# Kernel tuning notes

Hardware: AMD Instinct MI355X
Metric: run time of the kernel (lower is better)

The kernel has to match this reference:

```python
import jax, jax.numpy as jnp
import numpy as np

H = 1024      # hidden_size
NH = 16       # n_heads
DK = 64       # d_kv


def setup_inputs() -> dict:
    key = jax.random.key(0)
    k1, k2, k3, k4, k5 = jax.random.split(key, 5)
    x = jax.random.normal(k1, (4, 2048, H), dtype=jnp.float32)
    # dense1: hidden -> 3*n_heads*d_kv
    W1 = jax.random.normal(k2, (H, 3 * NH * DK), dtype=jnp.float32) / np.sqrt(H)
    b1 = jax.random.normal(k3, (3 * NH * DK,), dtype=jnp.float32) * 0.02
    # dense2: n_heads*d_kv -> hidden
    W2 = jax.random.normal(k4, (NH * DK, H), dtype=jnp.float32) / np.sqrt(NH * DK)
    b2 = jax.random.normal(k5, (H,), dtype=jnp.float32) * 0.02
    return {"x": x, "W1": W1, "b1": b1, "W2": W2, "b2": b2}


def reference(x, W1, b1, W2, b2):
    B, S, _ = x.shape
    scale = 1.0 / np.sqrt(DK)
    qkv = x @ W1 + b1                                   # [B,S,3*NH*DK]
    qkv = qkv.reshape(B, S, 3, NH, DK)
    q, k, v = jnp.moveaxis(qkv, 2, 0)                   # each [B,S,NH,DK]
    q = q.transpose(0, 2, 1, 3)                         # [B,NH,S,DK]
    k = k.transpose(0, 2, 1, 3)
    v = v.transpose(0, 2, 1, 3)
    scores = jnp.einsum('bhqd,bhkd->bhqk', q, k) * scale  # [B,NH,S,S]
    attn = jax.nn.softmax(scores, axis=-1)
    ctx = jnp.einsum('bhqk,bhkd->bhqd', attn, v)        # [B,NH,S,DK]
    ctx = ctx.transpose(0, 2, 1, 3).reshape(B, S, NH * DK)
    return ctx @ W2 + b2
```

## Files before the change

### kernel.cpp

```cpp
#include <hip/hip_runtime.h>
#include <hip/hip_bf16.h>


typedef __hip_bfloat16 bf16;
typedef __attribute__((ext_vector_type(8))) short bf16x8;
typedef __attribute__((ext_vector_type(4))) float f32x4;

#define B_   4
#define S_   2048
#define H_   1024
#define NH_  16
#define DK_  64
#define M_   8192
#define N1_  3072
#define K_   1024

#define SCALE_Q 0.18033688f

typedef const __attribute__((address_space(1))) void* gas_t;
typedef __attribute__((address_space(3))) void* las_t;
#define G2L16(g, l) __builtin_amdgcn_global_load_lds((gas_t)(g), (las_t)(l), 16, 0, 0)

__device__ __forceinline__ float b2f(bf16 v) { return __bfloat162float(v); }

__device__ __forceinline__ unsigned pk2(float a, float b) {
    unsigned ua = __float_as_uint(a);
    unsigned ub = __float_as_uint(b);
    ua += 0x7FFFu + ((ua >> 16) & 1u);
    ub += 0x7FFFu + ((ub >> 16) & 1u);
    return (ua >> 16) | (ub & 0xFFFF0000u);
}

__global__ __launch_bounds__(256) void conv_x(const float* __restrict__ X,
                                              bf16* __restrict__ Xb)
{
    size_t i = ((size_t)blockIdx.x * 256 + threadIdx.x) * 8;
    float4 lo = *(const float4*)&X[i];
    float4 hi = *(const float4*)&X[i + 4];
    uint4 u;
    u.x = pk2(lo.x, lo.y); u.y = pk2(lo.z, lo.w);
    u.z = pk2(hi.x, hi.y); u.w = pk2(hi.z, hi.w);
    *(uint4*)&Xb[i] = u;
}

__global__ __launch_bounds__(256) void conv_wT(const float* __restrict__ W,
                                               bf16* __restrict__ WT,
                                               int Kdim, int Ndim)
{
    __shared__ bf16 T[64][72];
    const int tid = threadIdx.x;
    const int n0 = blockIdx.x * 64, k0 = blockIdx.y * 64;
    const int kr = tid >> 4, nc = (tid & 15) * 4;
    #pragma unroll
    for (int p = 0; p < 4; ++p) {
        float4 v = *(const float4*)&W[(size_t)(k0 + kr + p * 16) * Ndim + n0 + nc];
        T[nc + 0][kr + p * 16] = __float2bfloat16(v.x);
        T[nc + 1][kr + p * 16] = __float2bfloat16(v.y);
        T[nc + 2][kr + p * 16] = __float2bfloat16(v.z);
        T[nc + 3][kr + p * 16] = __float2bfloat16(v.w);
    }
    __syncthreads();
    const int nr = tid >> 2, kc = (tid & 3) * 16;
    *(bf16x8*)&WT[(size_t)(n0 + nr) * Kdim + k0 + kc]     = *(const bf16x8*)&T[nr][kc];
    *(bf16x8*)&WT[(size_t)(n0 + nr) * Kdim + k0 + kc + 8] = *(const bf16x8*)&T[nr][kc + 8];
}

__device__ __forceinline__ void qkv_epilogue(
    const f32x4 acc[4][4], const float* __restrict__ B1,
    bf16* __restrict__ Qp, bf16* __restrict__ Kp, bf16* __restrict__ Vt,
    int n0, int m0, int wm, int wn, int quad, int col)
{
    const int which = n0 >> 10;
    const int bb = m0 >> 11;
    if (which == 2) {
        #pragma unroll
        for (int i = 0; i < 4; ++i) {
            int s = (m0 & (S_ - 1)) + wm * 64 + i * 16 + quad * 4;
            #pragma unroll
            for (int j = 0; j < 4; ++j) {
                int n = n0 + wn * 64 + j * 16 + col;
                int h = (n >> 6) & 15, d = n & 63;
                float bv = B1[n];
                uint2 t;
                t.x = pk2(acc[i][j][0] + bv, acc[i][j][1] + bv);
                t.y = pk2(acc[i][j][2] + bv, acc[i][j][3] + bv);
                *(uint2*)&Vt[(((size_t)(bb * NH_ + h)) * DK_ + d) * S_ + s] = t;
            }
        }
    } else {
        bf16* dst = which ? Kp : Qp;
        const float sc = which ? 1.0f : SCALE_Q;
        #pragma unroll
        for (int i = 0; i < 4; ++i) {
            #pragma unroll
            for (int r = 0; r < 4; ++r) {
                int s = (m0 & (S_ - 1)) + wm * 64 + i * 16 + quad * 4 + r;
                #pragma unroll
                for (int j = 0; j < 4; ++j) {
                    int n = n0 + wn * 64 + j * 16 + col;
                    int h = (n >> 6) & 15, d = n & 63;
                    dst[(((size_t)(bb * NH_ + h)) * S_ + s) * DK_ + d] =
                        __float2bfloat16((acc[i][j][r] + B1[n]) * sc);
                }
            }
        }
    }
}

__global__ __launch_bounds__(256) void gemm_qkv_mfma2(
    const bf16* __restrict__ Xb, const bf16* __restrict__ W1T,
    const float* __restrict__ B1,
    bf16* __restrict__ Qp, bf16* __restrict__ Kp, bf16* __restrict__ Vt)
{
    __shared__ bf16 As[128 * 32];
    __shared__ bf16 Bs[128 * 32];

    const int tid = threadIdx.x;
    const int lane = tid & 63, wv = tid >> 6;
    const int col = lane & 15, quad = lane >> 4;
    const int wm = wv >> 1, wn = wv & 1;
    const int n0 = blockIdx.x * 128, m0 = blockIdx.y * 128;

    f32x4 acc[4][4] = {};

    const bf16* Ag = Xb  + (size_t)m0 * K_;
    const bf16* Bg = W1T + (size_t)n0 * K_;

    for (int k0 = 0; k0 < K_; k0 += 32) {
        #pragma unroll
        for (int h = 0; h < 2; ++h) {
            int idx = tid + h * 256;
            int row = idx >> 2, c = (idx & 3) * 8;
            G2L16(Ag + (size_t)row * K_ + k0 + c, As + (size_t)idx * 8);
            G2L16(Bg + (size_t)row * K_ + k0 + c, Bs + (size_t)idx * 8);
        }
        __syncthreads();

        bf16x8 af[4], bfr[4];
        #pragma unroll
        for (int i = 0; i < 4; ++i)
            af[i] = *(const bf16x8*)&As[(wm * 64 + i * 16 + col) * 32 + quad * 8];
        #pragma unroll
        for (int j = 0; j < 4; ++j)
            bfr[j] = *(const bf16x8*)&Bs[(wn * 64 + j * 16 + col) * 32 + quad * 8];

        #pragma unroll
        for (int i = 0; i < 4; ++i)
            #pragma unroll
            for (int j = 0; j < 4; ++j)
                acc[i][j] = __builtin_amdgcn_mfma_f32_16x16x32_bf16(af[i], bfr[j], acc[i][j], 0, 0, 0);
        __syncthreads();
    }
    qkv_epilogue(acc, B1, Qp, Kp, Vt, n0, m0, wm, wn, quad, col);
}

__global__ __launch_bounds__(256) void gemm_qkv_mfma(
    const float* __restrict__ X, const bf16* __restrict__ W1T,
    const float* __restrict__ B1,
    bf16* __restrict__ Qp, bf16* __restrict__ Kp, bf16* __restrict__ Vt)
{
    __shared__ bf16 As[128 * 32];
    __shared__ bf16 Bs[128 * 32];

    const int tid = threadIdx.x;
    const int lane = tid & 63, wv = tid >> 6;
    const int col = lane & 15, quad = lane >> 4;
    const int wm = wv >> 1, wn = wv & 1;
    const int n0 = blockIdx.x * 128, m0 = blockIdx.y * 128;

    f32x4 acc[4][4] = {};

    const float* Ag = X   + (size_t)m0 * K_;
    const bf16*  Bg = W1T + (size_t)n0 * K_;

    for (int k0 = 0; k0 < K_; k0 += 32) {
        #pragma unroll
        for (int h = 0; h < 2; ++h) {
            int idx = tid + h * 256;
            int row = idx >> 2, c = (idx & 3) * 8;
            G2L16(Bg + (size_t)row * K_ + k0 + c, Bs + (size_t)idx * 8);
        }
        #pragma unroll
        for (int h = 0; h < 2; ++h) {
            int idx = tid + h * 256;
            int row = idx >> 2, c = (idx & 3) * 8;
            float4 lo = *(const float4*)&Ag[(size_t)row * K_ + k0 + c];
            float4 hi = *(const float4*)&Ag[(size_t)row * K_ + k0 + c + 4];
            uint4 u;
            u.x = pk2(lo.x, lo.y); u.y = pk2(lo.z, lo.w);
            u.z = pk2(hi.x, hi.y); u.w = pk2(hi.z, hi.w);
            *(uint4*)&As[(size_t)idx * 8] = u;
        }
        __syncthreads();

        bf16x8 af[4], bfr[4];
        #pragma unroll
        for (int i = 0; i < 4; ++i)
            af[i] = *(const bf16x8*)&As[(wm * 64 + i * 16 + col) * 32 + quad * 8];
        #pragma unroll
        for (int j = 0; j < 4; ++j)
            bfr[j] = *(const bf16x8*)&Bs[(wn * 64 + j * 16 + col) * 32 + quad * 8];

        #pragma unroll
        for (int i = 0; i < 4; ++i)
            #pragma unroll
            for (int j = 0; j < 4; ++j)
                acc[i][j] = __builtin_amdgcn_mfma_f32_16x16x32_bf16(af[i], bfr[j], acc[i][j], 0, 0, 0);
        __syncthreads();
    }
    qkv_epilogue(acc, B1, Qp, Kp, Vt, n0, m0, wm, wn, quad, col);
}

__global__ __launch_bounds__(512, 8) void attn_mfma(
    const bf16* __restrict__ Q, const bf16* __restrict__ K,
    const bf16* __restrict__ Vt, bf16* __restrict__ CTX)
{
    __shared__ bf16 Ks[64][72];
    __shared__ bf16 Vs[64][72];
    __shared__ bf16 Ps[8][16][72];

    const int tid  = threadIdx.x;
    const int wv   = tid >> 6;
    const int lane = tid & 63;
    const int col  = lane & 15;
    const int quad = lane >> 4;

    const int bh = blockIdx.y;
    const int q0 = blockIdx.x * 128;

    const bf16* Qg  = Q  + (size_t)bh * S_ * DK_;
    const bf16* Kg  = K  + (size_t)bh * S_ * DK_;
    const bf16* Vtg = Vt + (size_t)bh * DK_ * S_;

    const short oneb = (short)0x3F80;
    const bf16x8 ones = {oneb, oneb, oneb, oneb, oneb, oneb, oneb, oneb};

    const int qrow = q0 + wv * 16 + col;
    bf16x8 qf[2];
    qf[0] = *(const bf16x8*)&Qg[(size_t)qrow * DK_ + quad * 8];
    qf[1] = *(const bf16x8*)&Qg[(size_t)qrow * DK_ + 32 + quad * 8];

    f32x4 o[4] = {};
    f32x4 l_acc = {0.f, 0.f, 0.f, 0.f};

    const int sr = tid >> 3;
    const int e0 = (tid & 7) * 8;

    bf16x8 kreg = *(const bf16x8*)&Kg[(size_t)sr * DK_ + e0];
    bf16x8 vreg = *(const bf16x8*)&Vtg[(size_t)sr * S_ + e0];

    for (int kt = 0; kt < S_ / 64; ++kt) {
        *(bf16x8*)&Ks[sr][e0] = kreg;
        *(bf16x8*)&Vs[sr][e0] = vreg;
        __syncthreads();

        if (kt + 1 < S_ / 64) {
            kreg = *(const bf16x8*)&Kg[(size_t)((kt + 1) * 64 + sr) * DK_ + e0];
            vreg = *(const bf16x8*)&Vtg[(size_t)sr * S_ + (kt + 1) * 64 + e0];
        }

        #pragma unroll
        for (int cs = 0; cs < 4; ++cs) {
            const bf16* kb = &Ks[cs * 16 + col][0];
            f32x4 a = {0.f, 0.f, 0.f, 0.f};
            a = __builtin_amdgcn_mfma_f32_16x16x32_bf16(*(const bf16x8*)&kb[quad * 8],      qf[0], a, 0, 0, 0);
            a = __builtin_amdgcn_mfma_f32_16x16x32_bf16(*(const bf16x8*)&kb[32 + quad * 8], qf[1], a, 0, 0, 0);
            uint2 p;
            p.x = pk2(exp2f(a[0]), exp2f(a[1]));
            p.y = pk2(exp2f(a[2]), exp2f(a[3]));
            *(uint2*)&Ps[wv][col][cs * 16 + quad * 4] = p;
        }

        bf16x8 pf0 = *(const bf16x8*)&Ps[wv][col][quad * 8];
        bf16x8 pf1 = *(const bf16x8*)&Ps[wv][col][32 + quad * 8];

        l_acc = __builtin_amdgcn_mfma_f32_16x16x32_bf16(ones, pf0, l_acc, 0, 0, 0);
        l_acc = __builtin_amdgcn_mfma_f32_16x16x32_bf16(ones, pf1, l_acc, 0, 0, 0);

        #pragma unroll
        for (int ds = 0; ds < 4; ++ds) {
            const bf16* vb = &Vs[ds * 16 + col][0];
            o[ds] = __builtin_amdgcn_mfma_f32_16x16x32_bf16(*(const bf16x8*)&vb[quad * 8],      pf0, o[ds], 0, 0, 0);
            o[ds] = __builtin_amdgcn_mfma_f32_16x16x32_bf16(*(const bf16x8*)&vb[32 + quad * 8], pf1, o[ds], 0, 0, 0);
        }
        __syncthreads();
    }

    const int b = bh >> 4, h = bh & 15;
    const float inv = 1.f / l_acc[0];
    const int srow = q0 + wv * 16 + col;
    bf16* crow = CTX + ((size_t)(b * S_ + srow)) * H_ + h * DK_;
    #pragma unroll
    for (int ds = 0; ds < 4; ++ds) {
        uint2 t;
        t.x = pk2(o[ds][0] * inv, o[ds][1] * inv);
        t.y = pk2(o[ds][2] * inv, o[ds][3] * inv);
        *(uint2*)&crow[ds * 16 + quad * 4] = t;
    }
}

__global__ __launch_bounds__(256) void gemm_out_mfma(
    const bf16* __restrict__ Cx, const bf16* __restrict__ W2T,
    const float* __restrict__ B2, float* __restrict__ OUT)
{
    __shared__ bf16 As[128 * 32];
    __shared__ bf16 Bs[128 * 32];

    const int tid = threadIdx.x;
    const int lane = tid & 63, wv = tid >> 6;
    const int col = lane & 15, quad = lane >> 4;
    const int wm = wv >> 1, wn = wv & 1;
    const int n0 = blockIdx.x * 128, m0 = blockIdx.y * 128;

    f32x4 acc[4][4] = {};

    const bf16* Ag = Cx  + (size_t)m0 * K_;
    const bf16* Bg = W2T + (size_t)n0 * K_;

    for (int k0 = 0; k0 < K_; k0 += 32) {
        #pragma unroll
        for (int h = 0; h < 2; ++h) {
            int idx = tid + h * 256;
            int row = idx >> 2, c = (idx & 3) * 8;
            G2L16(Ag + (size_t)row * K_ + k0 + c, As + (size_t)idx * 8);
            G2L16(Bg + (size_t)row * K_ + k0 + c, Bs + (size_t)idx * 8);
        }
        __syncthreads();

        bf16x8 af[4], bfr[4];
        #pragma unroll
        for (int i = 0; i < 4; ++i)
            af[i] = *(const bf16x8*)&As[(wm * 64 + i * 16 + col) * 32 + quad * 8];
        #pragma unroll
        for (int j = 0; j < 4; ++j)
            bfr[j] = *(const bf16x8*)&Bs[(wn * 64 + j * 16 + col) * 32 + quad * 8];

        #pragma unroll
        for (int i = 0; i < 4; ++i)
            #pragma unroll
            for (int j = 0; j < 4; ++j)
                acc[i][j] = __builtin_amdgcn_mfma_f32_16x16x32_bf16(af[i], bfr[j], acc[i][j], 0, 0, 0);
        __syncthreads();
    }

    #pragma unroll
    for (int i = 0; i < 4; ++i) {
        #pragma unroll
        for (int r = 0; r < 4; ++r) {
            int m = m0 + wm * 64 + i * 16 + quad * 4 + r;
            #pragma unroll
            for (int j = 0; j < 4; ++j) {
                int n = n0 + wn * 64 + j * 16 + col;
                OUT[(size_t)m * H_ + n] = acc[i][j][r] + B2[n];
            }
        }
    }
}

extern "C" void kernel_launch(void* const* d_in, const int* in_sizes, int n_in,
                              void* d_out, int out_size, void* d_ws, size_t ws_size,
                              hipStream_t stream)
{
    const float* X  = (const float*)d_in[0];
    const float* W1 = (const float*)d_in[1];
    const float* B1 = (const float*)d_in[2];
    const float* W2 = (const float*)d_in[3];
    const float* B2 = (const float*)d_in[4];
    float* OUT = (float*)d_out;

    const size_t QE = (size_t)B_ * NH_ * S_ * DK_;
    bf16* Qw  = (bf16*)d_ws;
    bf16* Kw  = Qw + QE;
    bf16* Vw  = Kw + QE;
    bf16* Rw  = Vw + QE;
    bf16* W1T = Rw;
    bf16* Cw  = Rw;
    bf16* W2T = Qw;
    bf16* Xb  = Rw + QE;

    const bool fast = ws_size >= 5 * QE * sizeof(bf16);

    conv_wT<<<dim3(N1_ / 64, K_ / 64), 256, 0, stream>>>(W1, W1T, K_, N1_);
    if (fast) {
        conv_x<<<dim3((int)(QE / (256 * 8))), 256, 0, stream>>>(X, Xb);
        gemm_qkv_mfma2<<<dim3(N1_ / 128, M_ / 128), 256, 0, stream>>>(Xb, W1T, B1, Qw, Kw, Vw);
    } else {
        gemm_qkv_mfma<<<dim3(N1_ / 128, M_ / 128), 256, 0, stream>>>(X, W1T, B1, Qw, Kw, Vw);
    }
    attn_mfma<<<dim3(S_ / 128, B_ * NH_), 512, 0, stream>>>(Qw, Kw, Vw, Cw);
    conv_wT<<<dim3(H_ / 64, K_ / 64), 256, 0, stream>>>(W2, W2T, K_, H_);
    gemm_out_mfma<<<dim3(H_ / 128, M_ / 128), 256, 0, stream>>>(Cw, W2T, B2, OUT);
}
```

Baseline: 323.1 us.

## Process two query sub-tiles per wave in attention to reuse K/V fragments

```diff
diff --git a/kernel.cpp b/kernel.cpp
--- a/kernel.cpp
+++ b/kernel.cpp
@@ -211,13 +211,13 @@
     qkv_epilogue(acc, B1, Qp, Kp, Vt, n0, m0, wm, wn, quad, col);
 }
 
-__global__ __launch_bounds__(512, 8) void attn_mfma(
+__global__ __launch_bounds__(256, 4) void attn_mfma(
     const bf16* __restrict__ Q, const bf16* __restrict__ K,
     const bf16* __restrict__ Vt, bf16* __restrict__ CTX)
 {
     __shared__ bf16 Ks[64][72];
     __shared__ bf16 Vs[64][72];
-    __shared__ bf16 Ps[8][16][72];
+    __shared__ bf16 Ps[4][2][16][72];
 
     const int tid  = threadIdx.x;
     const int wv   = tid >> 6;
@@ -235,67 +235,92 @@
     const short oneb = (short)0x3F80;
     const bf16x8 ones = {oneb, oneb, oneb, oneb, oneb, oneb, oneb, oneb};
 
-    const int qrow = q0 + wv * 16 + col;
-    bf16x8 qf[2];
-    qf[0] = *(const bf16x8*)&Qg[(size_t)qrow * DK_ + quad * 8];
-    qf[1] = *(const bf16x8*)&Qg[(size_t)qrow * DK_ + 32 + quad * 8];
-
-    f32x4 o[4] = {};
-    f32x4 l_acc = {0.f, 0.f, 0.f, 0.f};
-
-    const int sr = tid >> 3;
-    const int e0 = (tid & 7) * 8;
-
-    bf16x8 kreg = *(const bf16x8*)&Kg[(size_t)sr * DK_ + e0];
-    bf16x8 vreg = *(const bf16x8*)&Vtg[(size_t)sr * S_ + e0];
+    bf16x8 qf[2][2];
+    #pragma unroll
+    for (int qs = 0; qs < 2; ++qs) {
+        const int qrow = q0 + wv * 32 + qs * 16 + col;
+        qf[qs][0] = *(const bf16x8*)&Qg[(size_t)qrow * DK_ + quad * 8];
+        qf[qs][1] = *(const bf16x8*)&Qg[(size_t)qrow * DK_ + 32 + quad * 8];
+    }
+
+    f32x4 o[2][4] = {};
+    f32x4 l_acc[2] = {};
+
+    const int sr = tid >> 2;
+    const int e0 = (tid & 3) * 16;
+
+    bf16x8 kreg0 = *(const bf16x8*)&Kg[(size_t)sr * DK_ + e0];
+    bf16x8 kreg1 = *(const bf16x8*)&Kg[(size_t)sr * DK_ + e0 + 8];
+    bf16x8 vreg0 = *(const bf16x8*)&Vtg[(size_t)sr * S_ + e0];
+    bf16x8 vreg1 = *(const bf16x8*)&Vtg[(size_t)sr * S_ + e0 + 8];
 
     for (int kt = 0; kt < S_ / 64; ++kt) {
-        *(bf16x8*)&Ks[sr][e0] = kreg;
-        *(bf16x8*)&Vs[sr][e0] = vreg;
+        *(bf16x8*)&Ks[sr][e0]     = kreg0;
+        *(bf16x8*)&Ks[sr][e0 + 8] = kreg1;
+        *(bf16x8*)&Vs[sr][e0]     = vreg0;
+        *(bf16x8*)&Vs[sr][e0 + 8] = vreg1;
         __syncthreads();
 
         if (kt + 1 < S_ / 64) {
-            kreg = *(const bf16x8*)&Kg[(size_t)((kt + 1) * 64 + sr) * DK_ + e0];
-            vreg = *(const bf16x8*)&Vtg[(size_t)sr * S_ + (kt + 1) * 64 + e0];
+            kreg0 = *(const bf16x8*)&Kg[(size_t)((kt + 1) * 64 + sr) * DK_ + e0];
+            kreg1 = *(const bf16x8*)&Kg[(size_t)((kt + 1) * 64 + sr) * DK_ + e0 + 8];
+            vreg0 = *(const bf16x8*)&Vtg[(size_t)sr * S_ + (kt + 1) * 64 + e0];
+            vreg1 = *(const bf16x8*)&Vtg[(size_t)sr * S_ + (kt + 1) * 64 + e0 + 8];
         }
 
         #pragma unroll
         for (int cs = 0; cs < 4; ++cs) {
             const bf16* kb = &Ks[cs * 16 + col][0];
-            f32x4 a = {0.f, 0.f, 0.f, 0.f};
-            a = __builtin_amdgcn_mfma_f32_16x16x32_bf16(*(const bf16x8*)&kb[quad * 8],      qf[0], a, 0, 0, 0);
-            a = __builtin_amdgcn_mfma_f32_16x16x32_bf16(*(const bf16x8*)&kb[32 + quad * 8], qf[1], a, 0, 0, 0);
-            uint2 p;
-            p.x = pk2(exp2f(a[0]), exp2f(a[1]));
-            p.y = pk2(exp2f(a[2]), exp2f(a[3]));
-            *(uint2*)&Ps[wv][col][cs * 16 + quad * 4] = p;
-        }
-
-        bf16x8 pf0 = *(const bf16x8*)&Ps[wv][col][quad * 8];
-        bf16x8 pf1 = *(const bf16x8*)&Ps[wv][col][32 + quad * 8];
-
-        l_acc = __builtin_amdgcn_mfma_f32_16x16x32_bf16(ones, pf0, l_acc, 0, 0, 0);
-        l_acc = __builtin_amdgcn_mfma_f32_16x16x32_bf16(ones, pf1, l_acc, 0, 0, 0);
+            bf16x8 ka0 = *(const bf16x8*)&kb[quad * 8];
+            bf16x8 ka1 = *(const bf16x8*)&kb[32 + quad * 8];
+            #pragma unroll
+            for (int qs = 0; qs < 2; ++qs) {
+                f32x4 a = {0.f, 0.f, 0.f, 0.f};
+                a = __builtin_amdgcn_mfma_f32_16x16x32_bf16(ka0, qf[qs][0], a, 0, 0, 0);
+                a = __builtin_amdgcn_mfma_f32_16x16x32_bf16(ka1, qf[qs][1], a, 0, 0, 0);
+                uint2 p;
+                p.x = pk2(exp2f(a[0]), exp2f(a[1]));
+                p.y = pk2(exp2f(a[2]), exp2f(a[3]));
+                *(uint2*)&Ps[wv][qs][col][cs * 16 + quad * 4] = p;
+            }
+        }
+
+        bf16x8 pf[2][2];
+        #pragma unroll
+        for (int qs = 0; qs < 2; ++qs) {
+            pf[qs][0] = *(const bf16x8*)&Ps[wv][qs][col][quad * 8];
+            pf[qs][1] = *(const bf16x8*)&Ps[wv][qs][col][32 + quad * 8];
+            l_acc[qs] = __builtin_amdgcn_mfma_f32_16x16x32_bf16(ones, pf[qs][0], l_acc[qs], 0, 0, 0);
+            l_acc[qs] = __builtin_amdgcn_mfma_f32_16x16x32_bf16(ones, pf[qs][1], l_acc[qs], 0, 0, 0);
+        }
 
         #pragma unroll
         for (int ds = 0; ds < 4; ++ds) {
             const bf16* vb = &Vs[ds * 16 + col][0];
-            o[ds] = __builtin_amdgcn_mfma_f32_16x16x32_bf16(*(const bf16x8*)&vb[quad * 8],      pf0, o[ds], 0, 0, 0);
-            o[ds] = __builtin_amdgcn_mfma_f32_16x16x32_bf16(*(const bf16x8*)&vb[32 + quad * 8], pf1, o[ds], 0, 0, 0);
+            bf16x8 va0 = *(const bf16x8*)&vb[quad * 8];
+            bf16x8 va1 = *(const bf16x8*)&vb[32 + quad * 8];
+            #pragma unroll
+            for (int qs = 0; qs < 2; ++qs) {
+                o[qs][ds] = __builtin_amdgcn_mfma_f32_16x16x32_bf16(va0, pf[qs][0], o[qs][ds], 0, 0, 0);
+                o[qs][ds] = __builtin_amdgcn_mfma_f32_16x16x32_bf16(va1, pf[qs][1], o[qs][ds], 0, 0, 0);
+            }
         }
         __syncthreads();
     }
 
     const int b = bh >> 4, h = bh & 15;
-    const float inv = 1.f / l_acc[0];
-    const int srow = q0 + wv * 16 + col;
-    bf16* crow = CTX + ((size_t)(b * S_ + srow)) * H_ + h * DK_;
     #pragma unroll
-    for (int ds = 0; ds < 4; ++ds) {
-        uint2 t;
-        t.x = pk2(o[ds][0] * inv, o[ds][1] * inv);
-        t.y = pk2(o[ds][2] * inv, o[ds][3] * inv);
-        *(uint2*)&crow[ds * 16 + quad * 4] = t;
+    for (int qs = 0; qs < 2; ++qs) {
+        const float inv = 1.f / l_acc[qs][0];
+        const int srow = q0 + wv * 32 + qs * 16 + col;
+        bf16* crow = CTX + ((size_t)(b * S_ + srow)) * H_ + h * DK_;
+        #pragma unroll
+        for (int ds = 0; ds < 4; ++ds) {
+            uint2 t;
+            t.x = pk2(o[qs][ds][0] * inv, o[qs][ds][1] * inv);
+            t.y = pk2(o[qs][ds][2] * inv, o[qs][ds][3] * inv);
+            *(uint2*)&crow[ds * 16 + quad * 4] = t;
+        }
     }
 }
 
@@ -387,7 +412,7 @@
     } else {
         gemm_qkv_mfma<<<dim3(N1_ / 128, M_ / 128), 256, 0, stream>>>(X, W1T, B1, Qw, Kw, Vw);
     }
-    attn_mfma<<<dim3(S_ / 128, B_ * NH_), 512, 0, stream>>>(Qw, Kw, Vw, Cw);
+    attn_mfma<<<dim3(S_ / 128, B_ * NH_), 256, 0, stream>>>(Qw, Kw, Vw, Cw);
     conv_wT<<<dim3(H_ / 64, K_ / 64), 256, 0, stream>>>(W2, W2T, K_, H_);
     gemm_out_mfma<<<dim3(H_ / 128, M_ / 128), 256, 0, stream>>>(Cw, W2T, B2, OUT);
 }
```

After: 319.9 us. About the same (-1.0%).
